# Optimization experiments

Hardware: AMD Instinct MI355X
Metric: run time of the kernel (lower is better)

The kernel has to match this reference:

```python
import jax, jax.numpy as jnp
import numpy as np

LN_EPS = 1e-5

def _moe_forward(x, Wg, bg, W1, b1, W2, b2, ln_w, ln_b, gate_scale, top_k=2):
    B, N, D = x.shape
    E = Wg.shape[1]
    x_flat = x.reshape(B * N, D)                      # [T, D]
    # --- router (MoEGate): softmax -> top-k -> renormalize ---
    logits = x_flat @ Wg + bg                         # [T, E]
    probs = jax.nn.softmax(logits, axis=-1)
    w, idx = jax.lax.top_k(probs, top_k)              # [T, k]
    w = w / jnp.sum(w, axis=-1, keepdims=True)
    # dense gate matrix [T, E]: scatter top-k weights onto their experts
    gates = jnp.sum(jax.nn.one_hot(idx, E, dtype=x.dtype) * w[..., None], axis=1)
    # --- experts: Linear -> GELU(erf) -> Linear, computed densely for all experts ---
    h = jax.nn.gelu(jnp.einsum('td,edo->eto', x_flat, W1) + b1[:, None, :],
                    approximate=False)                # [E, T, O]
    eo = jnp.einsum('eto,eoq->etq', h, W2) + b2[:, None, :]  # [E, T, O]
    # --- weighted combine (equivalent to masked scatter-add in the torch loop) ---
    out_flat = jnp.einsum('te,eto->to', gates, eo)    # [T, O]
    out = out_flat.reshape(B, N, -1) * gate_scale[0]
    # --- LayerNorm ---
    mu = jnp.mean(out, axis=-1, keepdims=True)
    var = jnp.var(out, axis=-1, keepdims=True)
    return (out - mu) / jnp.sqrt(var + LN_EPS) * ln_w + ln_b


def setup_inputs() -> dict:
    key = jax.random.key(0)
    ks = jax.random.split(key, 5)
    B, N, D, O, E = 8, 1024, 1024, 4096, 4
    return {
        'x': jax.random.normal(ks[0], (B, N, D), dtype=jnp.float32),
        'Wg': jax.random.normal(ks[1], (D, E), dtype=jnp.float32) * 0.02,
        'bg': jnp.zeros((E,), jnp.float32),
        'W1': jax.random.normal(ks[2], (E, D, O), dtype=jnp.float32) * (1.0 / np.sqrt(D)),
        'b1': jnp.zeros((E, O), jnp.float32),
        'W2': jax.random.normal(ks[3], (E, O, O), dtype=jnp.float32) * (1.0 / np.sqrt(O)),
        'b2': jnp.zeros((E, O), jnp.float32),
        'ln_w': jnp.ones((O,), jnp.float32),
        'ln_b': jnp.zeros((O,), jnp.float32),
        'gate_scale': jnp.ones((1,), jnp.float32) * 0.1,
    }


def reference(x, Wg, bg, W1, b1, W2, b2, ln_w, ln_b, gate_scale):
    return _moe_forward(x, Wg, bg, W1, b1, W2, b2, ln_w, ln_b, gate_scale)
```

## Files before the change

### kernel.cpp

```cpp
#include <hip/hip_runtime.h>
#include <cmath>


typedef float f32x4 __attribute__((ext_vector_type(4)));
typedef __bf16 bf16x8 __attribute__((ext_vector_type(8)));
typedef __bf16 bf16x4 __attribute__((ext_vector_type(4)));

#define T_TOK 8192
#define DDIM 1024
#define ODIM 4096
#define NEXP 4

__device__ __forceinline__ void gl_lds16(const void* g, void* l) {
    __builtin_amdgcn_global_load_lds(
        (const __attribute__((address_space(1))) void*)g,
        (__attribute__((address_space(3))) void*)l, 16, 0, 0);
}

__global__ __launch_bounds__(256) void cvt_bf16_vec(const float* __restrict__ in,
                                                    __bf16* __restrict__ out, int n4) {
    int i = blockIdx.x * 256 + threadIdx.x;
    if (i >= n4) return;
    float4 v = ((const float4*)in)[i];
    bf16x4 o = { (__bf16)v.x, (__bf16)v.y, (__bf16)v.z, (__bf16)v.w };
    ((bf16x4*)out)[i] = o;
}

__global__ __launch_bounds__(256) void transpose_cvt(const float* __restrict__ in,
                                                     __bf16* __restrict__ out,
                                                     int R, int C) {
    __shared__ float tile[32][33];
    const size_t eoff = (size_t)blockIdx.z * R * C;
    const float* ip = in + eoff;
    __bf16* op = out + eoff;
    const int c0 = blockIdx.x * 32, r0 = blockIdx.y * 32;
    const int tx = threadIdx.x, ty = threadIdx.y;
#pragma unroll
    for (int i = 0; i < 4; i++)
        tile[ty + i * 8][tx] = ip[(size_t)(r0 + ty + i * 8) * C + c0 + tx];
    __syncthreads();
#pragma unroll
    for (int i = 0; i < 4; i++)
        op[(size_t)(c0 + ty + i * 8) * R + r0 + tx] = (__bf16)tile[tx][ty + i * 8];
}

__global__ __launch_bounds__(256) void router_kernel(const float* __restrict__ x,
                                                     const float* __restrict__ Wg,
                                                     const float* __restrict__ bg,
                                                     int* __restrict__ counts,
                                                     int* __restrict__ perm,
                                                     float* __restrict__ wlist) {
    const int wave = threadIdx.x >> 6, lane = threadIdx.x & 63;
    const int t = blockIdx.x * 4 + wave;
    const float* xr = x + (size_t)t * DDIM;
    float a0 = 0.f, a1 = 0.f, a2 = 0.f, a3 = 0.f;
    const float4* Wg4 = (const float4*)Wg;
    for (int d = lane; d < DDIM; d += 64) {
        float xv = xr[d];
        float4 w = Wg4[d];
        a0 += xv * w.x; a1 += xv * w.y; a2 += xv * w.z; a3 += xv * w.w;
    }
#pragma unroll
    for (int off = 32; off; off >>= 1) {
        a0 += __shfl_xor(a0, off); a1 += __shfl_xor(a1, off);
        a2 += __shfl_xor(a2, off); a3 += __shfl_xor(a3, off);
    }
    if (lane == 0) {
        float l[4] = {a0 + bg[0], a1 + bg[1], a2 + bg[2], a3 + bg[3]};
        float mx = fmaxf(fmaxf(l[0], l[1]), fmaxf(l[2], l[3]));
        float p[4], s = 0.f;
#pragma unroll
        for (int e = 0; e < 4; e++) { p[e] = expf(l[e] - mx); s += p[e]; }
#pragma unroll
        for (int e = 0; e < 4; e++) p[e] /= s;
        int e1 = 0;
#pragma unroll
        for (int e = 1; e < 4; e++) if (p[e] > p[e1]) e1 = e;
        int e2 = (e1 == 0) ? 1 : 0;
#pragma unroll
        for (int e = 0; e < 4; e++) if (e != e1 && p[e] > p[e2]) e2 = e;
        const float inv = 1.0f / (p[e1] + p[e2]);
        int pos1 = atomicAdd(&counts[e1], 1);
        perm[e1 * T_TOK + pos1] = t;
        wlist[e1 * T_TOK + pos1] = p[e1] * inv;
        int pos2 = atomicAdd(&counts[e2], 1);
        perm[e2 * T_TOK + pos2] = t;
        wlist[e2 * T_TOK + pos2] = p[e2] * inv;
    }
}

template <int MODE, int KDIM>
__global__ __launch_bounds__(256) void moe_gemm(const __bf16* __restrict__ A,
                                                const __bf16* __restrict__ B,
                                                const float* __restrict__ bias,
                                                __bf16* __restrict__ Hout,
                                                float* __restrict__ Fout,
                                                const int* __restrict__ perm,
                                                const float* __restrict__ wlist,
                                                const int* __restrict__ countp) {
    constexpr int BK = 32;
    __shared__ __align__(16) __bf16 As[128 * BK];
    __shared__ __align__(16) __bf16 Bs[128 * BK];
    const int count = *countp;
    const int m0 = blockIdx.y * 128;
    if (m0 >= count) return;
    const int tid = threadIdx.x;
    const int wave = tid >> 6, lane = tid & 63;
    const int r16 = lane & 15, quad = lane >> 4;
    const int n0 = blockIdx.x * 128;
    const int wm = (wave & 1) * 64, wn = (wave >> 1) * 64;

    const int c0 = tid, c1 = tid + 256;
    const __bf16 *Ag0, *Ag1;
    if (MODE == 0) {
        Ag0 = A + (size_t)perm[m0 + (c0 >> 2)] * KDIM + (c0 & 3) * 8;
        Ag1 = A + (size_t)perm[m0 + (c1 >> 2)] * KDIM + (c1 & 3) * 8;
    } else {
        Ag0 = A + (size_t)(m0 + (c0 >> 2)) * KDIM + (c0 & 3) * 8;
        Ag1 = A + (size_t)(m0 + (c1 >> 2)) * KDIM + (c1 & 3) * 8;
    }
    const __bf16* Bg0 = B + (size_t)(n0 + (c0 >> 2)) * KDIM + (c0 & 3) * 8;
    const __bf16* Bg1 = B + (size_t)(n0 + (c1 >> 2)) * KDIM + (c1 & 3) * 8;
    __bf16* sA0 = &As[(wave * 64) * 8];
    __bf16* sA1 = &As[(256 + wave * 64) * 8];
    __bf16* sB0 = &Bs[(wave * 64) * 8];
    __bf16* sB1 = &Bs[(256 + wave * 64) * 8];

    f32x4 acc[4][4] = {};

    for (int k0 = 0; k0 < KDIM; k0 += BK) {
        gl_lds16(Ag0 + k0, sA0);
        gl_lds16(Ag1 + k0, sA1);
        gl_lds16(Bg0 + k0, sB0);
        gl_lds16(Bg1 + k0, sB1);
        __syncthreads();
        bf16x8 af[4], bfr[4];
#pragma unroll
        for (int i = 0; i < 4; i++)
            af[i] = *(const bf16x8*)&As[(wm + i * 16 + r16) * BK + quad * 8];
#pragma unroll
        for (int i = 0; i < 4; i++)
            bfr[i] = *(const bf16x8*)&Bs[(wn + i * 16 + r16) * BK + quad * 8];
#pragma unroll
        for (int mi = 0; mi < 4; mi++)
#pragma unroll
            for (int ni = 0; ni < 4; ni++)
                acc[mi][ni] = __builtin_amdgcn_mfma_f32_16x16x32_bf16(
                    af[mi], bfr[ni], acc[mi][ni], 0, 0, 0);
        __syncthreads();
    }

    const int colBase = n0 + wn + r16;
    if (MODE == 0) {
#pragma unroll
        for (int mi = 0; mi < 4; mi++) {
            const int rowBase = m0 + wm + mi * 16 + quad * 4;
#pragma unroll
            for (int ni = 0; ni < 4; ni++) {
                const int col = colBase + ni * 16;
                const float bv = bias[col];
#pragma unroll
                for (int r = 0; r < 4; r++) {
                    if (rowBase + r < count) {
                        float xv = acc[mi][ni][r] + bv;
                        float u = 1.5957691216057308f * xv * (1.0f + 0.044715f * xv * xv);
                        float gv = xv * __builtin_amdgcn_rcpf(1.0f + __expf(-u));
                        Hout[(size_t)(rowBase + r) * ODIM + col] = (__bf16)gv;
                    }
                }
            }
        }
    } else {
#pragma unroll
        for (int mi = 0; mi < 4; mi++) {
            const int rowBase = m0 + wm + mi * 16 + quad * 4;
            int tok[4]; float g[4]; bool ok[4];
#pragma unroll
            for (int r = 0; r < 4; r++) {
                const int i = rowBase + r;
                ok[r] = (i < count);
                tok[r] = ok[r] ? perm[i] : 0;
                g[r] = ok[r] ? wlist[i] : 0.f;
            }
#pragma unroll
            for (int ni = 0; ni < 4; ni++) {
                const int col = colBase + ni * 16;
                const float bv = bias[col];
#pragma unroll
                for (int r = 0; r < 4; r++) {
                    if (ok[r]) {
                        float v = g[r] * (acc[mi][ni][r] + bv);
                        Fout[(size_t)tok[r] * ODIM + col] += v;
                    }
                }
            }
        }
    }
}

__global__ __launch_bounds__(256) void ln_kernel(float* __restrict__ out,
                                                 const float* __restrict__ lw,
                                                 const float* __restrict__ lb,
                                                 const float* __restrict__ gsp) {
    const int t = blockIdx.x;
    float* row = out + (size_t)t * ODIM;
    const float gs = gsp[0];
    float4 v[4];
    float s = 0.f, ss = 0.f;
#pragma unroll
    for (int i = 0; i < 4; i++) {
        float4 a = ((const float4*)row)[threadIdx.x + i * 256];
        a.x *= gs; a.y *= gs; a.z *= gs; a.w *= gs;
        v[i] = a;
        s += a.x + a.y + a.z + a.w;
        ss += a.x * a.x + a.y * a.y + a.z * a.z + a.w * a.w;
    }
#pragma unroll
    for (int off = 32; off; off >>= 1) {
        s += __shfl_xor(s, off);
        ss += __shfl_xor(ss, off);
    }
    __shared__ float rs[4], rss[4];
    const int wave = threadIdx.x >> 6, lane = threadIdx.x & 63;
    if (lane == 0) { rs[wave] = s; rss[wave] = ss; }
    __syncthreads();
    s = rs[0] + rs[1] + rs[2] + rs[3];
    ss = rss[0] + rss[1] + rss[2] + rss[3];
    const float mu = s * (1.0f / ODIM);
    const float var = ss * (1.0f / ODIM) - mu * mu;
    const float inv = 1.0f / sqrtf(var + 1e-5f);
#pragma unroll
    for (int i = 0; i < 4; i++) {
        const int c4 = threadIdx.x + i * 256;
        float4 w4 = ((const float4*)lw)[c4];
        float4 b4 = ((const float4*)lb)[c4];
        float4 o;
        o.x = (v[i].x - mu) * inv * w4.x + b4.x;
        o.y = (v[i].y - mu) * inv * w4.y + b4.y;
        o.z = (v[i].z - mu) * inv * w4.z + b4.z;
        o.w = (v[i].w - mu) * inv * w4.w + b4.w;
        ((float4*)row)[c4] = o;
    }
}

extern "C" void kernel_launch(void* const* d_in, const int* in_sizes, int n_in,
                              void* d_out, int out_size, void* d_ws, size_t ws_size,
                              hipStream_t stream) {
    const float* x   = (const float*)d_in[0];
    const float* Wg  = (const float*)d_in[1];
    const float* bg  = (const float*)d_in[2];
    const float* W1  = (const float*)d_in[3];
    const float* b1  = (const float*)d_in[4];
    const float* W2  = (const float*)d_in[5];
    const float* b2  = (const float*)d_in[6];
    const float* lnw = (const float*)d_in[7];
    const float* lnb = (const float*)d_in[8];
    const float* gsc = (const float*)d_in[9];
    float* out = (float*)d_out;

    char* w = (char*)d_ws;
    __bf16* Xb  = (__bf16*)w;
    __bf16* W1T = Xb + (size_t)T_TOK * DDIM;
    __bf16* W2T = W1T + (size_t)NEXP * ODIM * DDIM;
    __bf16* H   = W2T + (size_t)NEXP * ODIM * ODIM;
    int*   counts = (int*)(H + (size_t)T_TOK * ODIM);
    int*   perm   = counts + NEXP;
    float* wlist  = (float*)(perm + NEXP * T_TOK);

    hipMemsetAsync(counts, 0, (NEXP + 2 * NEXP * T_TOK) * sizeof(int) , stream);
    hipMemsetAsync(out, 0, (size_t)T_TOK * ODIM * sizeof(float), stream);

    cvt_bf16_vec<<<(T_TOK * DDIM / 4) / 256, 256, 0, stream>>>(x, Xb, T_TOK * DDIM / 4);
    dim3 tb(32, 8);
    transpose_cvt<<<dim3(ODIM / 32, DDIM / 32, NEXP), tb, 0, stream>>>(W1, W1T, DDIM, ODIM);
    transpose_cvt<<<dim3(ODIM / 32, ODIM / 32, NEXP), tb, 0, stream>>>(W2, W2T, ODIM, ODIM);
    router_kernel<<<T_TOK / 4, 256, 0, stream>>>(x, Wg, bg, counts, perm, wlist);

    for (int e = 0; e < NEXP; e++) {
        moe_gemm<0, DDIM><<<dim3(ODIM / 128, T_TOK / 128), 256, 0, stream>>>(
            Xb, W1T + (size_t)e * ODIM * DDIM, b1 + e * ODIM,
            H, nullptr, perm + e * T_TOK, nullptr, counts + e);
        moe_gemm<1, ODIM><<<dim3(ODIM / 128, T_TOK / 128), 256, 0, stream>>>(
            H, W2T + (size_t)e * ODIM * ODIM, b2 + e * ODIM,
            nullptr, out, perm + e * T_TOK, wlist + e * T_TOK, counts + e);
    }
    ln_kernel<<<T_TOK, 256, 0, stream>>>(out, lnw, lnb, gsc);
}
```

Baseline: 2.049 ms.

## Replace MoE GEMM with 256x256 double-buffered swizzled-LDS kernel and XCD remap

Replaces the 128x128, BK=32 single-buffered expert GEMM with a 256x256 tile, BK=64 kernel using 512 threads. LDS is double-buffered with staggered global-to-LDS prefetch, and the LDS layout is XOR-swizzled to avoid bank conflicts. MFMA phases are interleaved with loads under s_setprio, and launched blocks are remapped linearly so that consecutive tiles land on the same XCD. The aim is higher arithmetic intensity and overlap of memory with MFMA, at the cost of more LDS and register pressure and more fragile hand-placed waitcnt and barrier logic.

```diff
diff --git a/kernel.cpp b/kernel.cpp
--- a/kernel.cpp
+++ b/kernel.cpp
@@ -89,80 +89,144 @@
     }
 }
 
+
+#define STAGE_A(t, h, bb)                                                      \
+  if ((t) < NT) {                                                              \
+    gl_lds16(pa##h##0 + (size_t)(t) * BK, &As[bb][h][w * 512]);                \
+    gl_lds16(pa##h##1 + (size_t)(t) * BK, &As[bb][h][w * 512 + 4096]);         \
+  }
+#define STAGE_B(t, h, bb)                                                      \
+  if ((t) < NT) {                                                              \
+    gl_lds16(pb##h##0 + (size_t)(t) * BK, &Bs[bb][h][w * 512]);                \
+    gl_lds16(pb##h##1 + (size_t)(t) * BK, &Bs[bb][h][w * 512 + 4096]);         \
+  }
+#define LDA(bb, mg, kk) (*(const bf16x8*)&As[bb][wr][(mg)*1024 + rowOff + offK##kk])
+#define LDB(bb, nn, kk) (*(const bf16x8*)&Bs[bb][wch][(nn)*1024 + rowBOff + offK##kk])
+#define MFMA4(p, nn)                                                           \
+  acc[2*(p)][nn]   = __builtin_amdgcn_mfma_f32_16x16x32_bf16(af0k0, bfr[nn][0], acc[2*(p)][nn], 0, 0, 0);   \
+  acc[2*(p)][nn]   = __builtin_amdgcn_mfma_f32_16x16x32_bf16(af0k1, bfr[nn][1], acc[2*(p)][nn], 0, 0, 0);   \
+  acc[2*(p)+1][nn] = __builtin_amdgcn_mfma_f32_16x16x32_bf16(af1k0, bfr[nn][0], acc[2*(p)+1][nn], 0, 0, 0); \
+  acc[2*(p)+1][nn] = __builtin_amdgcn_mfma_f32_16x16x32_bf16(af1k1, bfr[nn][1], acc[2*(p)+1][nn], 0, 0, 0);
+#define PHASE_TAIL(p)                                                          \
+  __builtin_amdgcn_s_barrier();                                                \
+  asm volatile("s_waitcnt lgkmcnt(0)" ::: "memory");                           \
+  __builtin_amdgcn_s_setprio(1);                                               \
+  MFMA4(p, 0) MFMA4(p, 1) MFMA4(p, 2) MFMA4(p, 3)                              \
+  __builtin_amdgcn_s_setprio(0);                                               \
+  __builtin_amdgcn_s_barrier();
+#define TILE(bb, t)                                                            \
+  {                                                                            \
+    bfr[0][0] = LDB(bb, 0, 0); bfr[0][1] = LDB(bb, 0, 1);                      \
+    bfr[1][0] = LDB(bb, 1, 0); bfr[1][1] = LDB(bb, 1, 1);                      \
+    bfr[2][0] = LDB(bb, 2, 0); bfr[2][1] = LDB(bb, 2, 1);                      \
+    bfr[3][0] = LDB(bb, 3, 0); bfr[3][1] = LDB(bb, 3, 1);                      \
+    af0k0 = LDA(bb, 0, 0); af0k1 = LDA(bb, 0, 1);                              \
+    af1k0 = LDA(bb, 1, 0); af1k1 = LDA(bb, 1, 1);                              \
+    STAGE_A((t) + 1, 0, (bb) ^ 1)                                              \
+    PHASE_TAIL(0)                                                              \
+    af0k0 = LDA(bb, 2, 0); af0k1 = LDA(bb, 2, 1);                              \
+    af1k0 = LDA(bb, 3, 0); af1k1 = LDA(bb, 3, 1);                              \
+    STAGE_A((t) + 1, 1, (bb) ^ 1)                                              \
+    PHASE_TAIL(1)                                                              \
+    af0k0 = LDA(bb, 4, 0); af0k1 = LDA(bb, 4, 1);                              \
+    af1k0 = LDA(bb, 5, 0); af1k1 = LDA(bb, 5, 1);                              \
+    STAGE_B((t) + 2, 0, bb)                                                    \
+    PHASE_TAIL(2)                                                              \
+    af0k0 = LDA(bb, 6, 0); af0k1 = LDA(bb, 6, 1);                              \
+    af1k0 = LDA(bb, 7, 0); af1k1 = LDA(bb, 7, 1);                              \
+    STAGE_B((t) + 2, 1, bb)                                                    \
+    if ((t) + 2 < NT) { asm volatile("s_waitcnt vmcnt(4)" ::: "memory"); }     \
+    else              { asm volatile("s_waitcnt vmcnt(0)" ::: "memory"); }     \
+    PHASE_TAIL(3)                                                              \
+  }
+
 template <int MODE, int KDIM>
-__global__ __launch_bounds__(256) void moe_gemm(const __bf16* __restrict__ A,
-                                                const __bf16* __restrict__ B,
-                                                const float* __restrict__ bias,
-                                                __bf16* __restrict__ Hout,
-                                                float* __restrict__ Fout,
-                                                const int* __restrict__ perm,
-                                                const float* __restrict__ wlist,
-                                                const int* __restrict__ countp) {
-    constexpr int BK = 32;
-    __shared__ __align__(16) __bf16 As[128 * BK];
-    __shared__ __align__(16) __bf16 Bs[128 * BK];
+__global__ __launch_bounds__(512, 2) void moe_gemm256(
+    const __bf16* __restrict__ A, const __bf16* __restrict__ B,
+    const float* __restrict__ bias, __bf16* __restrict__ Hout,
+    float* __restrict__ Fout, const int* __restrict__ perm,
+    const float* __restrict__ wlist, const int* __restrict__ countp) {
+    constexpr int BK = 64;
+    constexpr int NT = KDIM / BK;
+    constexpr int GX = ODIM / 256;
+
+    __shared__ __align__(16) __bf16 As[2][2][128 * 64];
+    __shared__ __align__(16) __bf16 Bs[2][2][128 * 64];
+
     const int count = *countp;
-    const int m0 = blockIdx.y * 128;
-    if (m0 >= count) return;
+    const int nAy = (count + 255) >> 8;
+    const int na = nAy * GX;
+    int lin = blockIdx.y * GX + blockIdx.x;
+    if (lin >= na) return;
+    {
+        const int q = na >> 3, r = na & 7;
+        const int xcd = lin & 7, loc = lin >> 3;
+        lin = xcd * q + (xcd < r ? xcd : r) + loc;
+    }
+    const int bx = lin & (GX - 1), by = lin / GX;
+    const int m0 = by * 256, n0 = bx * 256;
+
     const int tid = threadIdx.x;
-    const int wave = tid >> 6, lane = tid & 63;
+    const int w = tid >> 6, lane = tid & 63;
     const int r16 = lane & 15, quad = lane >> 4;
-    const int n0 = blockIdx.x * 128;
-    const int wm = (wave & 1) * 64, wn = (wave >> 1) * 64;
-
-    const int c0 = tid, c1 = tid + 256;
-    const __bf16 *Ag0, *Ag1;
+    const int wr = w >> 2;
+    const int wc = w & 3;
+    const int wch = wc >> 1;
+
+    const int swz = r16 & 7;
+    const int offK0 = ((quad) ^ swz) * 8;
+    const int offK1 = ((quad + 4) ^ swz) * 8;
+    const int rowOff = r16 * 64;
+    const int rowBOff = (wc & 1) * 4096 + rowOff;
+
+    const int srow = tid >> 3;
+    const int sq = ((tid & 7) ^ (srow & 7)) * 8;
+    const __bf16 *pa00, *pa01, *pa10, *pa11;
     if (MODE == 0) {
-        Ag0 = A + (size_t)perm[m0 + (c0 >> 2)] * KDIM + (c0 & 3) * 8;
-        Ag1 = A + (size_t)perm[m0 + (c1 >> 2)] * KDIM + (c1 & 3) * 8;
+        pa00 = A + (size_t)perm[m0 + srow] * KDIM + sq;
+        pa01 = A + (size_t)perm[m0 + 64 + srow] * KDIM + sq;
+        pa10 = A + (size_t)perm[m0 + 128 + srow] * KDIM + sq;
+        pa11 = A + (size_t)perm[m0 + 192 + srow] * KDIM + sq;
     } else {
-        Ag0 = A + (size_t)(m0 + (c0 >> 2)) * KDIM + (c0 & 3) * 8;
-        Ag1 = A + (size_t)(m0 + (c1 >> 2)) * KDIM + (c1 & 3) * 8;
-    }
-    const __bf16* Bg0 = B + (size_t)(n0 + (c0 >> 2)) * KDIM + (c0 & 3) * 8;
-    const __bf16* Bg1 = B + (size_t)(n0 + (c1 >> 2)) * KDIM + (c1 & 3) * 8;
-    __bf16* sA0 = &As[(wave * 64) * 8];
-    __bf16* sA1 = &As[(256 + wave * 64) * 8];
-    __bf16* sB0 = &Bs[(wave * 64) * 8];
-    __bf16* sB1 = &Bs[(256 + wave * 64) * 8];
-
-    f32x4 acc[4][4] = {};
-
-    for (int k0 = 0; k0 < KDIM; k0 += BK) {
-        gl_lds16(Ag0 + k0, sA0);
-        gl_lds16(Ag1 + k0, sA1);
-        gl_lds16(Bg0 + k0, sB0);
-        gl_lds16(Bg1 + k0, sB1);
-        __syncthreads();
-        bf16x8 af[4], bfr[4];
-#pragma unroll
-        for (int i = 0; i < 4; i++)
-            af[i] = *(const bf16x8*)&As[(wm + i * 16 + r16) * BK + quad * 8];
-#pragma unroll
-        for (int i = 0; i < 4; i++)
-            bfr[i] = *(const bf16x8*)&Bs[(wn + i * 16 + r16) * BK + quad * 8];
-#pragma unroll
-        for (int mi = 0; mi < 4; mi++)
-#pragma unroll
-            for (int ni = 0; ni < 4; ni++)
-                acc[mi][ni] = __builtin_amdgcn_mfma_f32_16x16x32_bf16(
-                    af[mi], bfr[ni], acc[mi][ni], 0, 0, 0);
-        __syncthreads();
-    }
-
-    const int colBase = n0 + wn + r16;
+        pa00 = A + (size_t)(m0 + srow) * KDIM + sq;
+        pa01 = A + (size_t)(m0 + 64 + srow) * KDIM + sq;
+        pa10 = A + (size_t)(m0 + 128 + srow) * KDIM + sq;
+        pa11 = A + (size_t)(m0 + 192 + srow) * KDIM + sq;
+    }
+    const __bf16* pb00 = B + (size_t)(n0 + srow) * KDIM + sq;
+    const __bf16* pb01 = B + (size_t)(n0 + 64 + srow) * KDIM + sq;
+    const __bf16* pb10 = B + (size_t)(n0 + 128 + srow) * KDIM + sq;
+    const __bf16* pb11 = B + (size_t)(n0 + 192 + srow) * KDIM + sq;
+
+    f32x4 acc[8][4] = {};
+    bf16x8 bfr[4][2];
+    bf16x8 af0k0, af0k1, af1k0, af1k1;
+
+    STAGE_B(0, 0, 0) STAGE_B(0, 1, 0)
+    STAGE_A(0, 0, 0) STAGE_A(0, 1, 0)
+    STAGE_B(1, 0, 1) STAGE_B(1, 1, 1)
+    asm volatile("s_waitcnt vmcnt(4)" ::: "memory");
+    __builtin_amdgcn_s_barrier();
+
+    for (int t = 0; t < NT; t += 2) {
+        TILE(0, t)
+        TILE(1, t + 1)
+    }
+
+    const int colBase = n0 + wc * 64 + r16;
+    const int rowW = m0 + wr * 128 + quad * 4;
     if (MODE == 0) {
 #pragma unroll
-        for (int mi = 0; mi < 4; mi++) {
-            const int rowBase = m0 + wm + mi * 16 + quad * 4;
-#pragma unroll
-            for (int ni = 0; ni < 4; ni++) {
-                const int col = colBase + ni * 16;
+        for (int mg = 0; mg < 8; mg++) {
+            const int rowBase = rowW + mg * 16;
+#pragma unroll
+            for (int n = 0; n < 4; n++) {
+                const int col = colBase + n * 16;
                 const float bv = bias[col];
 #pragma unroll
                 for (int r = 0; r < 4; r++) {
                     if (rowBase + r < count) {
-                        float xv = acc[mi][ni][r] + bv;
+                        float xv = acc[mg][n][r] + bv;
                         float u = 1.5957691216057308f * xv * (1.0f + 0.044715f * xv * xv);
                         float gv = xv * __builtin_amdgcn_rcpf(1.0f + __expf(-u));
                         Hout[(size_t)(rowBase + r) * ODIM + col] = (__bf16)gv;
@@ -172,8 +236,8 @@
         }
     } else {
 #pragma unroll
-        for (int mi = 0; mi < 4; mi++) {
-            const int rowBase = m0 + wm + mi * 16 + quad * 4;
+        for (int mg = 0; mg < 8; mg++) {
+            const int rowBase = rowW + mg * 16;
             int tok[4]; float g[4]; bool ok[4];
 #pragma unroll
             for (int r = 0; r < 4; r++) {
@@ -183,13 +247,13 @@
                 g[r] = ok[r] ? wlist[i] : 0.f;
             }
 #pragma unroll
-            for (int ni = 0; ni < 4; ni++) {
-                const int col = colBase + ni * 16;
+            for (int n = 0; n < 4; n++) {
+                const int col = colBase + n * 16;
                 const float bv = bias[col];
 #pragma unroll
                 for (int r = 0; r < 4; r++) {
                     if (ok[r]) {
-                        float v = g[r] * (acc[mi][ni][r] + bv);
+                        float v = g[r] * (acc[mg][n][r] + bv);
                         Fout[(size_t)tok[r] * ODIM + col] += v;
                     }
                 }
@@ -197,6 +261,14 @@
         }
     }
 }
+
+#undef STAGE_A
+#undef STAGE_B
+#undef LDA
+#undef LDB
+#undef MFMA4
+#undef PHASE_TAIL
+#undef TILE
 
 __global__ __launch_bounds__(256) void ln_kernel(float* __restrict__ out,
                                                  const float* __restrict__ lw,
@@ -277,10 +349,10 @@
     router_kernel<<<T_TOK / 4, 256, 0, stream>>>(x, Wg, bg, counts, perm, wlist);
 
     for (int e = 0; e < NEXP; e++) {
-        moe_gemm<0, DDIM><<<dim3(ODIM / 128, T_TOK / 128), 256, 0, stream>>>(
+        moe_gemm256<0, DDIM><<<dim3(ODIM / 256, T_TOK / 256), 512, 0, stream>>>(
             Xb, W1T + (size_t)e * ODIM * DDIM, b1 + e * ODIM,
             H, nullptr, perm + e * T_TOK, nullptr, counts + e);
-        moe_gemm<1, ODIM><<<dim3(ODIM / 128, T_TOK / 128), 256, 0, stream>>>(
+        moe_gemm256<1, ODIM><<<dim3(ODIM / 256, T_TOK / 256), 512, 0, stream>>>(
             H, W2T + (size_t)e * ODIM * ODIM, b2 + e * ODIM,
             nullptr, out, perm + e * T_TOK, wlist + e * T_TOK, counts + e);
     }
```

New measurement: 2.234 ms. 9.1% more time.
